# Performance work log

Hardware: AMD Instinct MI355X
Metric: run time of the kernel (lower is better)

Reference implementation:

```python
import jax, jax.numpy as jnp
import numpy as np

N_HEADS = 16
N_KV = 8
HEAD_DIM = 128
HID = 2048
GROUPS = N_HEADS // N_KV
THETA = 10000.0


def _rope_cos_sin(position_ids, dtype):
    # position_ids: [1, S] int
    inv_freq = 1.0 / (THETA ** (jnp.arange(0, HEAD_DIM, 2, dtype=jnp.float32) / HEAD_DIM))
    freqs = position_ids.astype(jnp.float32)[:, :, None] * inv_freq[None, None, :]  # [1,S,hd/2]
    emb = jnp.concatenate([freqs, freqs], axis=-1)  # [1,S,hd]
    return jnp.cos(emb).astype(dtype)[:, None, :, :], jnp.sin(emb).astype(dtype)[:, None, :, :]


def _rotate_half(x):
    x1, x2 = x[..., : HEAD_DIM // 2], x[..., HEAD_DIM // 2 :]
    return jnp.concatenate([-x2, x1], axis=-1)


def setup_inputs() -> dict:
    key = jax.random.key(0)
    ks = jax.random.split(key, 8)
    B, S = 2, 2048
    hidden_states = jax.random.normal(ks[0], (B, S, HID), jnp.float32)
    Wq = jax.random.normal(ks[1], (HID, N_HEADS * HEAD_DIM), jnp.float32) * 0.02
    Wk = jax.random.normal(ks[2], (HID, N_KV * HEAD_DIM), jnp.float32) * 0.02
    Wv = jax.random.normal(ks[3], (HID, N_KV * HEAD_DIM), jnp.float32) * 0.02
    Wo = jax.random.normal(ks[4], (HID, HID), jnp.float32) * 0.02
    gate = jnp.zeros((1, N_HEADS, 1, 1), jnp.float32)
    memory_in = jax.random.normal(ks[5], (B, N_KV, HEAD_DIM, HEAD_DIM), jnp.float32)
    norm_in = jax.random.uniform(ks[6], (B, N_KV, 1, HEAD_DIM), jnp.float32)
    position_ids = jnp.arange(S, dtype=jnp.int32)[None, :]
    return {"hidden_states": hidden_states, "Wq": Wq, "Wk": Wk, "Wv": Wv, "Wo": Wo,
            "gate": gate, "memory_in": memory_in, "norm_in": norm_in,
            "position_ids": position_ids}


def reference(hidden_states, Wq, Wk, Wv, Wo, gate, memory_in, norm_in, position_ids):
    B, S, _ = hidden_states.shape
    # projections -> [B, H, S, hd]
    q = jnp.einsum('bsh,ho->bso', hidden_states, Wq).reshape(B, S, N_HEADS, HEAD_DIM).transpose(0, 2, 1, 3)
    k = jnp.einsum('bsh,ho->bso', hidden_states, Wk).reshape(B, S, N_KV, HEAD_DIM).transpose(0, 2, 1, 3)
    v = jnp.einsum('bsh,ho->bso', hidden_states, Wv).reshape(B, S, N_KV, HEAD_DIM).transpose(0, 2, 1, 3)

    # ---- compressive memory retrieval (pre-RoPE q, as in original) ----
    sigma_q = jax.nn.elu(q) + 1.0  # [B, nH, S, hd]
    mem_tiled = jnp.tile(memory_in, (1, GROUPS, 1, 1))          # torch .repeat tiles
    norm_tiled = jnp.tile(norm_in, (1, GROUPS, 1, 1))            # [B, nH, 1, hd]
    memory_output = jnp.einsum('bhsd,bhde->bhse', sigma_q, mem_tiled)
    norm_bcast = jnp.einsum('bhsd,bhd->bhs', sigma_q, norm_tiled[:, :, 0, :])[..., None]
    memory_output = memory_output / norm_bcast

    # ---- memory update (pre-RoPE k, v) ----
    sigma_k = jax.nn.elu(k) + 1.0  # [B, nKV, S, hd]
    updated_memory = memory_in + jnp.einsum('bhsd,bhse->bhde', sigma_k, v)
    updated_norm = norm_in + jnp.sum(sigma_k, axis=2, keepdims=True)

    # ---- RoPE ----
    cos, sin = _rope_cos_sin(position_ids, q.dtype)
    q = q * cos + _rotate_half(q) * sin
    k = k * cos + _rotate_half(k) * sin

    # ---- repeat_kv (interleave, groups) ----
    k = jnp.repeat(k, GROUPS, axis=1)
    v = jnp.repeat(v, GROUPS, axis=1)

    # ---- causal SDPA ----
    scale = 1.0 / np.sqrt(HEAD_DIM)
    scores = jnp.einsum('bhqd,bhkd->bhqk', q, k) * scale
    causal = jnp.tril(jnp.ones((S, S), dtype=bool))
    scores = jnp.where(causal[None, None], scores, jnp.finfo(scores.dtype).min)
    probs = jax.nn.softmax(scores, axis=-1)
    attn = jnp.einsum('bhqk,bhkd->bhqd', probs, v)

    # ---- gated combination + output projection ----
    g = jax.nn.sigmoid(gate)
    combined = g * memory_output + (1.0 - g) * attn  # [B, nH, S, hd]
    combined = combined.transpose(0, 2, 1, 3).reshape(B, S, HID)
    final_output = jnp.einsum('bsh,ho->bso', combined, Wo)
    return final_output, updated_memory, updated_norm
```

## Files before the change

kernel.cpp:

```cpp
#include <hip/hip_runtime.h>

#define BATCH 2
#define SEQ   2048
#define HID   2048
#define NH    16
#define NKV   8
#define HD    128
#define M_ROWS (BATCH * SEQ)
#define QKV_N  4096

typedef __attribute__((ext_vector_type(8))) __bf16 bf16x8;
typedef __attribute__((ext_vector_type(4))) float  f32x4;

static __device__ __forceinline__ f32x4 mfma16(bf16x8 a, bf16x8 b, f32x4 c) {
    return __builtin_amdgcn_mfma_f32_16x16x32_bf16(a, b, c, 0, 0, 0);
}
static __device__ __forceinline__ float sigma_f(float x) {
    return x > 0.f ? x + 1.f : __expf(x);
}
static __device__ __forceinline__ void gload16(const __bf16* g, __bf16* l) {
    __builtin_amdgcn_global_load_lds(
        (const __attribute__((address_space(1))) void*)g,
        (__attribute__((address_space(3))) void*)l, 16, 0, 0);
}

#define OFF_QKV  0ull
#define OFF_SQ   67108864ull
#define OFF_QR   83886080ull
#define OFF_KR   100663296ull
#define OFF_VT   109051904ull
#define OFF_ND   117440512ull
#define OFF_CB   117702656ull
#define OFF_PART 134479872ull
#define OFF_BND  142868480ull
#define OFF_MAXP 143130624ull
#define OFF_NPART 143134720ull
#define NSPLIT 8

__global__ __launch_bounds__(256) void pre_k(const float* __restrict__ hidden,
                                             const float* __restrict__ Wq,
                                             const float* __restrict__ Wk,
                                             const float* __restrict__ Wv,
                                             __bf16* __restrict__ hb,
                                             __bf16* __restrict__ qkvT)
{
    __shared__ __bf16 T[64][72];
    const int bid = blockIdx.x;
    const int t = threadIdx.x;
    if (bid < 4096) {
        const size_t i = ((size_t)bid * 256 + t) * 8;
        const float4 v0 = *reinterpret_cast<const float4*>(hidden + i);
        const float4 v1 = *reinterpret_cast<const float4*>(hidden + i + 4);
        bf16x8 o;
        o[0]=(__bf16)v0.x; o[1]=(__bf16)v0.y; o[2]=(__bf16)v0.z; o[3]=(__bf16)v0.w;
        o[4]=(__bf16)v1.x; o[5]=(__bf16)v1.y; o[6]=(__bf16)v1.z; o[7]=(__bf16)v1.w;
        *reinterpret_cast<bf16x8*>(hb + i) = o;
        return;
    }
    int tb = bid - 4096;
    const float* W; __bf16* Bt; int N;
    if (tb < 1024)      { W = Wq; Bt = qkvT;                         N = 2048; }
    else if (tb < 1536) { W = Wk; Bt = qkvT + (size_t)2048 * HID;    N = 1024; tb -= 1024; }
    else                { W = Wv; Bt = qkvT + (size_t)3072 * HID;    N = 1024; tb -= 1536; }
    const int k0 = (tb & 31) * 64, n0 = (tb >> 5) * 64;
    #pragma unroll
    for (int i = 0; i < 4; ++i) {
        const int idx = t + i * 256;
        const int r = idx >> 4, c4 = (idx & 15) * 4;
        const float4 v = *reinterpret_cast<const float4*>(&W[(size_t)(k0 + r) * N + n0 + c4]);
        T[c4 + 0][r] = (__bf16)v.x; T[c4 + 1][r] = (__bf16)v.y;
        T[c4 + 2][r] = (__bf16)v.z; T[c4 + 3][r] = (__bf16)v.w;
    }
    __syncthreads();
    #pragma unroll
    for (int i = 0; i < 2; ++i) {
        const int idx = t + i * 256;
        const int rr = idx >> 3, cc = (idx & 7) * 8;
        *reinterpret_cast<bf16x8*>(&Bt[(size_t)(n0 + rr) * HID + k0 + cc]) =
            *reinterpret_cast<bf16x8*>(&T[rr][cc]);
    }
}

__global__ __launch_bounds__(256) void tr_k(const float* __restrict__ W,
                                            __bf16* __restrict__ Bt, int K, int N)
{
    __shared__ __bf16 T[64][72];
    const int k0 = blockIdx.x * 64, n0 = blockIdx.y * 64;
    const int t = threadIdx.x;
    #pragma unroll
    for (int i = 0; i < 4; ++i) {
        const int idx = t + i * 256;
        const int r = idx >> 4, c4 = (idx & 15) * 4;
        const float4 v = *reinterpret_cast<const float4*>(&W[(size_t)(k0 + r) * N + n0 + c4]);
        T[c4 + 0][r] = (__bf16)v.x; T[c4 + 1][r] = (__bf16)v.y;
        T[c4 + 2][r] = (__bf16)v.z; T[c4 + 3][r] = (__bf16)v.w;
    }
    __syncthreads();
    #pragma unroll
    for (int i = 0; i < 2; ++i) {
        const int idx = t + i * 256;
        const int rr = idx >> 3, cc = (idx & 7) * 8;
        *reinterpret_cast<bf16x8*>(&Bt[(size_t)(n0 + rr) * K + k0 + cc]) =
            *reinterpret_cast<bf16x8*>(&T[rr][cc]);
    }
}

__global__ __launch_bounds__(512, 2) void gemm8_k(const __bf16* __restrict__ A,
                                                  const __bf16* __restrict__ Bt,
                                                  float* __restrict__ C,
                                                  int N, int K)
{
    __shared__ __align__(16) __bf16 smem[65536];
    const int tid = threadIdx.x, wave = tid >> 6, lane = tid & 63;
    const int l15 = lane & 15, l4 = lane >> 4;
    const int wr = wave >> 2, wc = wave & 3;

    const int nwg = gridDim.x;
    const int swz = (blockIdx.x & 7) * (nwg >> 3) + (blockIdx.x >> 3);
    const int NBN = N >> 8;
    const int bm = swz / NBN, bn = swz - bm * NBN;
    const int m0 = bm << 8, n0 = bn << 8;

    const int NKT = K >> 6;

    const int srow   = tid >> 2;
    const int schunk = (tid & 3) ^ ((tid >> 3) & 3);
    const int sdst   = wave * 512;

    const int achunk = l4 ^ ((l15 >> 1) & 3);
    const int aoff = (wr * 128 + l15) * 32 + achunk * 8;
    const int boff = (wc * 64  + l15) * 32 + achunk * 8;

    f32x4 acc[2][4][4] = {};
    bf16x8 af[4], bfr[4];

#define STAGE_SLAB(gb, r0, koff, slabptr) do {                                   \
        const __bf16* _g = (gb) + (size_t)((r0) + srow) * K + (koff) + schunk * 8; \
        gload16(_g,                    (slabptr) + sdst);                        \
        gload16(_g + (size_t)128 * K,  (slabptr) + sdst + 4096);                 \
    } while (0)

    STAGE_SLAB(A,  m0, 0,  smem);
    STAGE_SLAB(Bt, n0, 0,  smem + 16384);
    STAGE_SLAB(A,  m0, 32, smem + 8192);
    STAGE_SLAB(Bt, n0, 32, smem + 24576);
    STAGE_SLAB(A,  m0, 64, smem + 32768);
    STAGE_SLAB(Bt, n0, 64, smem + 32768 + 16384);
    asm volatile("s_waitcnt vmcnt(4)" ::: "memory");
    __builtin_amdgcn_s_barrier();

    #pragma unroll 1
    for (int T = 0; T < NKT; ++T) {
        __bf16* bufc = smem + (T & 1) * 32768;
        __bf16* bufn = smem + ((T & 1) ^ 1) * 32768;
        const int kt1 = (T + 1) * 64, kt2 = (T + 2) * 64;

        {
            const __bf16* As = bufc;
            const __bf16* Bs = bufc + 16384;
            #pragma unroll
            for (int f = 0; f < 4; ++f)  af[f]  = *reinterpret_cast<const bf16x8*>(As + aoff + f * 512);
            #pragma unroll
            for (int nf = 0; nf < 4; ++nf) bfr[nf] = *reinterpret_cast<const bf16x8*>(Bs + boff + nf * 512);
            if (T + 1 < NKT) STAGE_SLAB(A, m0, kt1 + 32, bufn + 8192);
            __builtin_amdgcn_s_barrier();
            __builtin_amdgcn_s_setprio(1);
            #pragma unroll
            for (int f = 0; f < 4; ++f)
                #pragma unroll
                for (int nf = 0; nf < 4; ++nf)
                    acc[0][f][nf] = mfma16(af[f], bfr[nf], acc[0][f][nf]);
            __builtin_amdgcn_s_setprio(0);
            __builtin_amdgcn_s_barrier();
        }
        {
            const __bf16* As = bufc;
            #pragma unroll
            for (int f = 0; f < 4; ++f)  af[f] = *reinterpret_cast<const bf16x8*>(As + aoff + 2048 + f * 512);
            if (T + 1 < NKT) STAGE_SLAB(Bt, n0, kt1 + 32, bufn + 24576);
            __builtin_amdgcn_s_barrier();
            __builtin_amdgcn_s_setprio(1);
            #pragma unroll
            for (int f = 0; f < 4; ++f)
                #pragma unroll
                for (int nf = 0; nf < 4; ++nf)
                    acc[1][f][nf] = mfma16(af[f], bfr[nf], acc[1][f][nf]);
            __builtin_amdgcn_s_setprio(0);
            __builtin_amdgcn_s_barrier();
        }
        {
            const __bf16* As = bufc + 8192;
            const __bf16* Bs = bufc + 24576;
            #pragma unroll
            for (int f = 0; f < 4; ++f)  af[f]  = *reinterpret_cast<const bf16x8*>(As + aoff + f * 512);
            #pragma unroll
            for (int nf = 0; nf < 4; ++nf) bfr[nf] = *reinterpret_cast<const bf16x8*>(Bs + boff + nf * 512);
            if (T + 2 < NKT) STAGE_SLAB(A, m0, kt2, bufc);
            __builtin_amdgcn_s_barrier();
            __builtin_amdgcn_s_setprio(1);
            #pragma unroll
            for (int f = 0; f < 4; ++f)
                #pragma unroll
                for (int nf = 0; nf < 4; ++nf)
                    acc[0][f][nf] = mfma16(af[f], bfr[nf], acc[0][f][nf]);
            __builtin_amdgcn_s_setprio(0);
            __builtin_amdgcn_s_barrier();
        }
        {
            const __bf16* As = bufc + 8192;
            #pragma unroll
            for (int f = 0; f < 4; ++f)  af[f] = *reinterpret_cast<const bf16x8*>(As + aoff + 2048 + f * 512);
            if (T + 2 < NKT) STAGE_SLAB(Bt, n0, kt2, bufc + 16384);
            __builtin_amdgcn_s_barrier();
            __builtin_amdgcn_s_setprio(1);
            #pragma unroll
            for (int f = 0; f < 4; ++f)
                #pragma unroll
                for (int nf = 0; nf < 4; ++nf)
                    acc[1][f][nf] = mfma16(af[f], bfr[nf], acc[1][f][nf]);
            __builtin_amdgcn_s_setprio(0);
            if (T < NKT - 2) asm volatile("s_waitcnt vmcnt(4)" ::: "memory");
            else             asm volatile("s_waitcnt vmcnt(0)" ::: "memory");
            __builtin_amdgcn_s_barrier();
        }
    }
#undef STAGE_SLAB

    #pragma unroll
    for (int mh = 0; mh < 2; ++mh)
        #pragma unroll
        for (int f = 0; f < 4; ++f)
            #pragma unroll
            for (int nf = 0; nf < 4; ++nf)
                #pragma unroll
                for (int r = 0; r < 4; ++r) {
                    const int row = m0 + wr * 128 + mh * 64 + f * 16 + l4 * 4 + r;
                    const int col = n0 + wc * 64 + nf * 16 + l15;
                    C[(size_t)row * N + col] = acc[mh][f][nf][r];
                }
}

__global__ __launch_bounds__(512, 2) void gemm8n_k(const __bf16* __restrict__ A,
                                                   const __bf16* __restrict__ Bt,
                                                   float* __restrict__ C,
                                                   int N, int K)
{
    __shared__ __align__(16) __bf16 smem[49152];
    const int tid = threadIdx.x, wave = tid >> 6, lane = tid & 63;
    const int l15 = lane & 15, l4 = lane >> 4;
    const int wr = wave >> 2, wc = wave & 3;

    const int nwg = gridDim.x;
    const int swz = (blockIdx.x & 7) * (nwg >> 3) + (blockIdx.x >> 3);
    const int NBN = N >> 8;
    const int bm = swz / NBN, bn = swz - bm * NBN;
    const int m0 = bm << 7, n0 = bn << 8;

    const int NKT = K >> 6;

    const int srow   = tid >> 2;
    const int schunk = (tid & 3) ^ ((tid >> 3) & 3);
    const int sdst   = wave * 512;

    const int achunk = l4 ^ ((l15 >> 1) & 3);
    const int aoff = (wr * 64 + l15) * 32 + achunk * 8;
    const int boff = (wc * 64 + l15) * 32 + achunk * 8;

    f32x4 acc[4][4] = {};
    bf16x8 af[4], bfr[4];

#define STAGE_A(koff, dstp) do {                                                  \
        gload16(A + (size_t)(m0 + srow) * K + (koff) + schunk * 8, (dstp) + sdst); \
    } while (0)
#define STAGE_B(koff, dstp) do {                                                  \
        const __bf16* _g = Bt + (size_t)(n0 + srow) * K + (koff) + schunk * 8;    \
        gload16(_g,                   (dstp) + sdst);                             \
        gload16(_g + (size_t)128 * K, (dstp) + sdst + 4096);                      \
    } while (0)

    STAGE_A(0,  smem);
    STAGE_B(0,  smem + 8192);
    STAGE_A(32, smem + 4096);
    STAGE_B(32, smem + 16384);
    STAGE_A(64, smem + 24576);
    STAGE_B(64, smem + 24576 + 8192);
    asm volatile("s_waitcnt vmcnt(3)" ::: "memory");
    __builtin_amdgcn_s_barrier();

    #pragma unroll 1
    for (int T = 0; T < NKT; ++T) {
        __bf16* bufc = smem + (T & 1) * 24576;
        __bf16* bufn = smem + ((T & 1) ^ 1) * 24576;
        const int kt1 = (T + 1) * 64, kt2 = (T + 2) * 64;

        {
            #pragma unroll
            for (int f = 0; f < 4; ++f)  af[f]  = *reinterpret_cast<const bf16x8*>(bufc + aoff + f * 512);
            #pragma unroll
            for (int nf = 0; nf < 4; ++nf) bfr[nf] = *reinterpret_cast<const bf16x8*>(bufc + 8192 + boff + nf * 512);
            if (T + 1 < NKT) { STAGE_A(kt1 + 32, bufn + 4096); STAGE_B(kt1 + 32, bufn + 16384); }
            __builtin_amdgcn_s_barrier();
            __builtin_amdgcn_s_setprio(1);
            #pragma unroll
            for (int f = 0; f < 4; ++f)
                #pragma unroll
                for (int nf = 0; nf < 4; ++nf)
                    acc[f][nf] = mfma16(af[f], bfr[nf], acc[f][nf]);
            __builtin_amdgcn_s_setprio(0);
            __builtin_amdgcn_s_barrier();
        }
        {
            #pragma unroll
            for (int f = 0; f < 4; ++f)  af[f]  = *reinterpret_cast<const bf16x8*>(bufc + 4096 + aoff + f * 512);
            #pragma unroll
            for (int nf = 0; nf < 4; ++nf) bfr[nf] = *reinterpret_cast<const bf16x8*>(bufc + 16384 + boff + nf * 512);
            if (T + 2 < NKT) { STAGE_A(kt2, bufc); STAGE_B(kt2, bufc + 8192); }
            __builtin_amdgcn_s_barrier();
            __builtin_amdgcn_s_setprio(1);
            #pragma unroll
            for (int f = 0; f < 4; ++f)
                #pragma unroll
                for (int nf = 0; nf < 4; ++nf)
                    acc[f][nf] = mfma16(af[f], bfr[nf], acc[f][nf]);
            __builtin_amdgcn_s_setprio(0);
            if (T < NKT - 2) asm volatile("s_waitcnt vmcnt(3)" ::: "memory");
            else             asm volatile("s_waitcnt vmcnt(0)" ::: "memory");
            __builtin_amdgcn_s_barrier();
        }
    }
#undef STAGE_A
#undef STAGE_B

    #pragma unroll
    for (int f = 0; f < 4; ++f)
        #pragma unroll
        for (int nf = 0; nf < 4; ++nf)
            #pragma unroll
            for (int r = 0; r < 4; ++r) {
                const int row = m0 + wr * 64 + f * 16 + l4 * 4 + r;
                const int col = n0 + wc * 64 + nf * 16 + l15;
                C[(size_t)row * N + col] = acc[f][nf][r];
            }
}

__global__ __launch_bounds__(256) void prep_k(const float* __restrict__ qkv,
                                              const float* __restrict__ norm_in,
                                              const int* __restrict__ pos_ids,
                                              __bf16* __restrict__ sq, __bf16* __restrict__ qr,
                                              __bf16* __restrict__ kr, __bf16* __restrict__ vt,
                                              float* __restrict__ nd, float* __restrict__ bnd,
                                              float* __restrict__ maxp)
{
    const int sc = blockIdx.x, kvh = blockIdx.y, b = blockIdx.z;
    const int s0 = sc * 32, t = threadIdx.x;
    const float scale = 0.08838834764831845f;
    const float s2 = scale * scale;
    const float NEG_LN_TH = -0.14391156831212787f;
    __shared__ float krn[32];

    {
        const int row = t >> 2;
        const int head = row >> 5, sl = row & 31;
        const int hq = kvh * 2 + head, nh = hq & 7;
        const int dq = (t & 3) * 16;
        const int pos = pos_ids[s0 + sl];
        const float* qp = qkv + (size_t)(b * SEQ + s0 + sl) * QKV_N + hq * 128;
        const float* np = norm_in + (b * NKV + nh) * 128;

        float x0[16], x1[16];
        #pragma unroll
        for (int i = 0; i < 16; i += 4) {
            *reinterpret_cast<float4*>(&x0[i]) = *reinterpret_cast<const float4*>(qp + dq + i);
            *reinterpret_cast<float4*>(&x1[i]) = *reinterpret_cast<const float4*>(qp + dq + 64 + i);
        }
        float nds = 0.f, qns = 0.f;
        bf16x8 sqv0[2], sqv1[2], qrv0[2], qrv1[2];
        #pragma unroll
        for (int i = 0; i < 16; ++i) {
            const int j = dq + i;
            float c, sn;
            __sincosf((float)pos * __expf((float)j * NEG_LN_TH), &sn, &c);
            qrv0[i >> 3][i & 7] = (__bf16)((x0[i] * c - x1[i] * sn) * scale);
            qrv1[i >> 3][i & 7] = (__bf16)((x1[i] * c + x0[i] * sn) * scale);
            const float sg0 = sigma_f(x0[i]), sg1 = sigma_f(x1[i]);
            sqv0[i >> 3][i & 7] = (__bf16)sg0;
            sqv1[i >> 3][i & 7] = (__bf16)sg1;
            nds += sg0 * np[j] + sg1 * np[j + 64];
            qns += (x0[i] * x0[i] + x1[i] * x1[i]) * s2;
        }
        __bf16* sqp = sq + ((size_t)(b * NH + hq) * SEQ + s0 + sl) * 128;
        __bf16* qrp = qr + ((size_t)(b * NH + hq) * SEQ + s0 + sl) * 128;
        *reinterpret_cast<bf16x8*>(sqp + dq)      = sqv0[0];
        *reinterpret_cast<bf16x8*>(sqp + dq + 8)  = sqv0[1];
        *reinterpret_cast<bf16x8*>(sqp + dq + 64) = sqv1[0];
        *reinterpret_cast<bf16x8*>(sqp + dq + 72) = sqv1[1];
        *reinterpret_cast<bf16x8*>(qrp + dq)      = qrv0[0];
        *reinterpret_cast<bf16x8*>(qrp + dq + 8)  = qrv0[1];
        *reinterpret_cast<bf16x8*>(qrp + dq + 64) = qrv1[0];
        *reinterpret_cast<bf16x8*>(qrp + dq + 72) = qrv1[1];

        nds += __shfl_xor(nds, 1); nds += __shfl_xor(nds, 2);
        qns += __shfl_xor(qns, 1); qns += __shfl_xor(qns, 2);
        if ((t & 3) == 0) {
            nd [(size_t)(b * NH + hq) * SEQ + s0 + sl] = nds;
            bnd[(size_t)(b * NH + hq) * SEQ + s0 + sl] = qns;
        }
    }

    if (t < 128) {
        const int sl = t >> 2;
        const int dq = (t & 3) * 16;
        const int pos = pos_ids[s0 + sl];
        const float* kp = qkv + (size_t)(b * SEQ + s0 + sl) * QKV_N + 2048 + kvh * 128;
        float x0[16], x1[16];
        #pragma unroll
        for (int i = 0; i < 16; i += 4) {
            *reinterpret_cast<float4*>(&x0[i]) = *reinterpret_cast<const float4*>(kp + dq + i);
            *reinterpret_cast<float4*>(&x1[i]) = *reinterpret_cast<const float4*>(kp + dq + 64 + i);
        }
        bf16x8 kv0[2], kv1[2];
        float kns = 0.f;
        #pragma unroll
        for (int i = 0; i < 16; ++i) {
            const int j = dq + i;
            float c, sn;
            __sincosf((float)pos * __expf((float)j * NEG_LN_TH), &sn, &c);
            kv0[i >> 3][i & 7] = (__bf16)(x0[i] * c - x1[i] * sn);
            kv1[i >> 3][i & 7] = (__bf16)(x1[i] * c + x0[i] * sn);
            kns += x0[i] * x0[i] + x1[i] * x1[i];
        }
        __bf16* krp = kr + ((size_t)(b * NKV + kvh) * SEQ + s0 + sl) * 128;
        *reinterpret_cast<bf16x8*>(krp + dq)      = kv0[0];
        *reinterpret_cast<bf16x8*>(krp + dq + 8)  = kv0[1];
        *reinterpret_cast<bf16x8*>(krp + dq + 64) = kv1[0];
        *reinterpret_cast<bf16x8*>(krp + dq + 72) = kv1[1];
        kns += __shfl_xor(kns, 1); kns += __shfl_xor(kns, 2);
        if ((t & 3) == 0) krn[sl] = kns;
    }

    __shared__ float vl[128][33];
    {
        const int sl = t >> 3, dch = (t & 7) * 16;
        const float* vp = qkv + (size_t)(b * SEQ + s0 + sl) * QKV_N + 3072 + kvh * 128 + dch;
        float xv[16];
        #pragma unroll
        for (int i = 0; i < 16; i += 4)
            *reinterpret_cast<float4*>(&xv[i]) = *reinterpret_cast<const float4*>(vp + i);
        #pragma unroll
        for (int i = 0; i < 16; ++i) vl[dch + i][sl] = xv[i];
    }
    __syncthreads();
    if (t == 0) {
        float mx = 0.f;
        #pragma unroll
        for (int i = 0; i < 32; ++i) mx = fmaxf(mx, krn[i]);
        maxp[((b * NKV + kvh) << 6) + sc] = mx;
    }
    {
        const int d = t >> 1, sh = (t & 1) * 16;
        bf16x8 o0, o1;
        #pragma unroll
        for (int j = 0; j < 8; ++j) o0[j] = (__bf16)vl[d][sh + j];
        #pragma unroll
        for (int j = 0; j < 8; ++j) o1[j] = (__bf16)vl[d][sh + 8 + j];
        __bf16* vp = vt + ((size_t)((b * NKV + kvh) * 128 + d)) * SEQ + s0 + sh;
        *reinterpret_cast<bf16x8*>(vp)     = o0;
        *reinterpret_cast<bf16x8*>(vp + 8) = o1;
    }
}

__global__ __launch_bounds__(256) void memout_k(const __bf16* __restrict__ sq,
                                                const float* __restrict__ mem_in,
                                                const float* __restrict__ nd,
                                                const float* __restrict__ gate,
                                                __bf16* __restrict__ cb)
{
    __shared__ __align__(16) __bf16 mt[128][136];
    const int tid = threadIdx.x;
    const int h = blockIdx.y, b = blockIdx.z;
    const int s0 = blockIdx.x * 64;

    const float* mem = mem_in + (size_t)(b * NKV + (h & 7)) * 16384;
    for (int i = tid; i < 16384; i += 256) {
        int dd = i >> 7, e = i & 127;
        mt[e][dd] = (__bf16)mem[i];
    }
    __syncthreads();

    const int wave = tid >> 6, lane = tid & 63, l15 = lane & 15, l4 = lane >> 4;
    f32x4 acc[8] = {};
    const __bf16* sqb = sq + ((size_t)(b * NH + h) * SEQ + s0 + wave * 16 + l15) * 128;
    #pragma unroll
    for (int kb = 0; kb < 4; ++kb) {
        bf16x8 a = *reinterpret_cast<const bf16x8*>(sqb + kb * 32 + l4 * 8);
        #pragma unroll
        for (int nc = 0; nc < 8; ++nc) {
            bf16x8 bb = *reinterpret_cast<bf16x8*>(&mt[nc * 16 + l15][kb * 32 + l4 * 8]);
            acc[nc] = mfma16(a, bb, acc[nc]);
        }
    }
    float g = 1.f / (1.f + __expf(-gate[h]));
    #pragma unroll
    for (int r = 0; r < 4; ++r) {
        int srow = s0 + wave * 16 + l4 * 4 + r;
        float scl = g / nd[(size_t)(b * NH + h) * SEQ + srow];
        __bf16* cbp = cb + (size_t)(b * SEQ + srow) * HID + h * 128;
        #pragma unroll
        for (int nc = 0; nc < 8; ++nc)
            cbp[nc * 16 + l15] = (__bf16)(acc[nc][r] * scl);
    }
}

__global__ __launch_bounds__(256) void memupd_k(const float* __restrict__ qkv,
                                                float* __restrict__ part,
                                                float* __restrict__ npart)
{
    const int sp = blockIdx.x, yy = blockIdx.y, b = blockIdx.z;
    const int h = yy & 7, eh = yy >> 3;
    const int tid = threadIdx.x;
    const int tx = tid & 15, ty = tid >> 4;
    __shared__ __align__(16) float sk[8][128];
    __shared__ __align__(16) float sv[8][64];
    float acc[8][4] = {};
    float nacc = 0.f;

    const int s0 = sp * (SEQ / NSPLIT);
    for (int so = 0; so < SEQ / NSPLIT; so += 8) {
        for (int i = tid; i < 8 * 128; i += 256) {
            int rr = i >> 7, dd = i & 127;
            sk[rr][dd] = sigma_f(qkv[(size_t)(b * SEQ + s0 + so + rr) * QKV_N + 2048 + h * 128 + dd]);
        }
        {
            const int rr = tid >> 6, ee = tid & 63;
            const size_t base = (size_t)(b * SEQ + s0 + so) * QKV_N + 3072 + h * 128 + eh * 64 + ee;
            sv[rr][ee]     = qkv[base + (size_t)rr * QKV_N];
            sv[rr + 4][ee] = qkv[base + (size_t)(rr + 4) * QKV_N];
        }
        __syncthreads();
        if (eh == 0 && tid < 128) {
            #pragma unroll
            for (int rr = 0; rr < 8; ++rr) nacc += sk[rr][tid];
        }
        #pragma unroll
        for (int rr = 0; rr < 8; ++rr) {
            float4 k0 = *reinterpret_cast<float4*>(&sk[rr][tx * 8]);
            float4 k1 = *reinterpret_cast<float4*>(&sk[rr][tx * 8 + 4]);
            float4 v0 = *reinterpret_cast<float4*>(&sv[rr][ty * 4]);
            float kreg[8] = {k0.x,k0.y,k0.z,k0.w,k1.x,k1.y,k1.z,k1.w};
            float vreg[4] = {v0.x,v0.y,v0.z,v0.w};
            #pragma unroll
            for (int i = 0; i < 8; ++i)
                #pragma unroll
                for (int j2 = 0; j2 < 4; ++j2)
                    acc[i][j2] += kreg[i] * vreg[j2];
        }
        __syncthreads();
    }
    float* pb = part + ((size_t)sp * (BATCH * NKV) + b * NKV + h) * 16384;
    #pragma unroll
    for (int i = 0; i < 8; ++i) {
        float4 o; o.x = acc[i][0]; o.y = acc[i][1]; o.z = acc[i][2]; o.w = acc[i][3];
        *reinterpret_cast<float4*>(&pb[(tx * 8 + i) * 128 + eh * 64 + ty * 4]) = o;
    }
    if (eh == 0 && tid < 128)
        npart[((size_t)sp * (BATCH * NKV) + b * NKV + h) * 128 + tid] = nacc;
}

__global__ __launch_bounds__(256) void memrednorm_k(const float* __restrict__ part,
                                                    const float* __restrict__ mem_in,
                                                    float* __restrict__ out_mem,
                                                    const float* __restrict__ npart,
                                                    const float* __restrict__ norm_in,
                                                    float* __restrict__ out_norm)
{
    const int bid = blockIdx.x;
    if (bid < 1024) {
        const size_t i = (size_t)bid * 256 + threadIdx.x;
        float a = mem_in[i];
        #pragma unroll
        for (int sp = 0; sp < NSPLIT; ++sp) a += part[(size_t)sp * 262144 + i];
        out_mem[i] = a;
    } else if (threadIdx.x < 128) {
        const int bh = bid - 1024, d = threadIdx.x;
        float a = norm_in[bh * 128 + d];
        #pragma unroll
        for (int sp = 0; sp < NSPLIT; ++sp)
            a += npart[((size_t)sp * (BATCH * NKV) + bh) * 128 + d];
        out_norm[bh * 128 + d] = a;
    }
}

__global__ __launch_bounds__(256, 2) void attn_k(const __bf16* __restrict__ qr,
                                                 const __bf16* __restrict__ kr,
                                                 const __bf16* __restrict__ vt,
                                                 const float* __restrict__ gate,
                                                 const float* __restrict__ bnd,
                                                 const float* __restrict__ maxp,
                                                 __bf16* __restrict__ cb)
{
    __shared__ __align__(16) char smem[81920];
    char* ksB = smem;
    char* vsB = smem + 32768;
    char* pB  = smem + 65536;
    float*  red  = (float*)smem;
    float*  lred = (float*)(smem + 65536);

    const int tid = threadIdx.x, wave = tid >> 6, lane = tid & 63;
    const int l15 = lane & 15, l4 = lane >> 4;
    const int e3 = l15 & 7, e2 = e3 >> 2;
    const int ksub = wave >> 1;
    const int wq   = wave & 1;

    const int n   = blockIdx.x + 16 * (blockIdx.y + 16 * blockIdx.z);
    const int xcd = n & 7, i64 = n >> 3;
    const int grp = xcd * 2 + (i64 >> 5);
    const int within = i64 & 31;
    const int b   = grp >> 3;
    const int kvh = grp & 7;
    const int h   = kvh * 2 + (within >> 4);
    const int x   = within & 15;

    const __bf16* kbase = kr + (size_t)(b * NKV + kvh) * SEQ * 128;
    const __bf16* vbase = vt + (size_t)(b * NKV + kvh) * 128 * SEQ;
    const float* bbase  = bnd + (size_t)(b * NH + h) * SEQ;

    const float g  = 1.f / (1.f + __expf(-gate[h]));
    const float gi = 1.f - g;
    float kn2 = 0.f;
    const float* mp = maxp + (b * NKV + kvh) * 64;
    #pragma unroll
    for (int i = 0; i < 64; i += 4) {
        const float4 v = *reinterpret_cast<const float4*>(mp + i);
        kn2 = fmaxf(kn2, fmaxf(fmaxf(v.x, v.y), fmaxf(v.z, v.w)));
    }
    const float knmax = sqrtf(kn2);

    bf16x8 ones;
    #pragma unroll
    for (int j = 0; j < 8; ++j) ones[j] = (__bf16)1.0f;

    const int srow = wave * 32 + l4;
    const int chA  = (lane & 15) ^ l4;
    const char* KG0 = (const char*)kbase + srow * 256 + chA * 16;
    const char* KG1 = (const char*)kbase + srow * 256 + ((chA ^ 4) * 16);
    const char* VG0 = (const char*)vbase + srow * 4096 + chA * 16;
    const char* VG1 = (const char*)vbase + srow * 4096 + ((chA ^ 4) * 16);
    __bf16* kdst = (__bf16*)(ksB + wave * 8192);
    __bf16* vdst = (__bf16*)(vsB + wave * 8192);

    const int t16 = (l4 ^ (e3 & 3)) * 16;
    const int KBe = l15 * 256 + ksub * 16384 + t16 + e2 * 64;
    const int KBo = l15 * 256 + ksub * 16384 + t16 + (1 ^ e2) * 64;
    const int VB0 = l15 * 256 + t16 + e2 * 64 + ksub * 128;
    const int VB1 = l15 * 256 + t16 + (1 ^ e2) * 64 + ksub * 128;
    const int PWw = wave * 4096 + l4 * 512 + l15 * 2;
    const int PWr = wave * 4096 + l15 * 128 + l4 * 16;

#define ISSUE_K(ktrow) do {                                                      \
        const int _ko = (ktrow) * 256;                                           \
        _Pragma("unroll")                                                        \
        for (int _j = 0; _j < 8; ++_j)                                           \
            gload16((const __bf16*)(((_j & 1) ? KG1 : KG0) + _ko + _j * 1024),   \
                    kdst + _j * 512);                                            \
    } while (0)
#define ISSUE_V(ktrow) do {                                                      \
        const int _vo = (ktrow) * 2;                                             \
        _Pragma("unroll")                                                        \
        for (int _j = 0; _j < 8; ++_j)                                           \
            gload16((const __bf16*)(((_j & 1) ? VG1 : VG0) + _vo + _j * 16384),  \
                    vdst + _j * 512);                                            \
    } while (0)

    #pragma unroll 1
    for (int tile = 0; tile < 2; ++tile) {
        const int q0 = (tile == 0 ? x : 31 - x) * 64;
        const int qw = q0 + wq * 32;
        const int NT = (q0 >> 6) + 1;
        const int NI = (NT + 1) >> 1;

        bf16x8 af[2][4];
        float m_r[2][4];
        #pragma unroll
        for (int m = 0; m < 2; ++m) {
            const __bf16* qb = qr + ((size_t)(b * NH + h) * SEQ + qw + m * 16 + l15) * 128;
            #pragma unroll
            for (int kb = 0; kb < 4; ++kb)
                af[m][kb] = *reinterpret_cast<const bf16x8*>(qb + kb * 32 + l4 * 8);
            #pragma unroll
            for (int r = 0; r < 4; ++r)
                m_r[m][r] = sqrtf(bbase[qw + m * 16 + l4 * 4 + r]) * knmax + 1.0f;
        }

        f32x4 o0[8] = {}, o1[8] = {};
        f32x4 lc0 = {}, lc1 = {};

        ISSUE_K(0);
        ISSUE_V(0);
        asm volatile("s_waitcnt vmcnt(8)" ::: "memory");
        __builtin_amdgcn_sched_barrier(0);
        __builtin_amdgcn_s_barrier();

        #pragma unroll 1
        for (int it = 0; it < NI; ++it) {
            const int s = 2 * it + ksub;
            const bool act  = (s < NT);
            const bool more = (it + 1 < NI);

            f32x4 s0[4] = {}, s1[4] = {};
            if (act) {
                __builtin_amdgcn_s_setprio(1);
                #pragma unroll
                for (int kb = 0; kb < 4; ++kb) {
                    const int kbb = ((kb & 1) ? KBo : KBe) + (kb >> 1) * 128;
                    #pragma unroll
                    for (int sub = 0; sub < 4; ++sub) {
                        bf16x8 bb = *reinterpret_cast<const bf16x8*>(ksB + kbb + sub * 4096);
                        s0[sub] = mfma16(af[0][kb], bb, s0[sub]);
                        s1[sub] = mfma16(af[1][kb], bb, s1[sub]);
                    }
                }
                __builtin_amdgcn_s_setprio(0);
            }
            __builtin_amdgcn_sched_barrier(0);
            __builtin_amdgcn_s_barrier();

            if (more) ISSUE_K((it + 1) * 128);

            if (act) {
                #pragma unroll
                for (int r = 0; r < 4; ++r) {
                    const int q0r = qw + l4 * 4 + r;
                    const int q1r = q0r + 16;
                    #pragma unroll
                    for (int sub = 0; sub < 4; ++sub) {
                        const int key = s * 64 + sub * 16 + l15;
                        float p0 = __expf(s0[sub][r] - m_r[0][r]);
                        float p1 = __expf(s1[sub][r] - m_r[1][r]);
                        p0 = (key <= q0r) ? p0 : 0.f;
                        p1 = (key <= q1r) ? p1 : 0.f;
                        *(__bf16*)(pB + PWw + r * 128 + sub * 32)        = (__bf16)p0;
                        *(__bf16*)(pB + PWw + 2048 + r * 128 + sub * 32) = (__bf16)p1;
                    }
                }
            }
            if (more) asm volatile("s_waitcnt vmcnt(8)" ::: "memory");
            else      asm volatile("s_waitcnt vmcnt(0)" ::: "memory");
            __builtin_amdgcn_sched_barrier(0);
            __builtin_amdgcn_s_barrier();

            if (act) {
                bf16x8 a00 = *reinterpret_cast<const bf16x8*>(pB + PWr);
                bf16x8 a01 = *reinterpret_cast<const bf16x8*>(pB + PWr + 64);
                bf16x8 a10 = *reinterpret_cast<const bf16x8*>(pB + PWr + 2048);
                bf16x8 a11 = *reinterpret_cast<const bf16x8*>(pB + PWr + 2048 + 64);
                __builtin_amdgcn_s_setprio(1);
                lc0 = mfma16(a00, ones, lc0); lc0 = mfma16(a01, ones, lc0);
                lc1 = mfma16(a10, ones, lc1); lc1 = mfma16(a11, ones, lc1);
                #pragma unroll
                for (int nc = 0; nc < 8; ++nc) {
                    bf16x8 b0 = *reinterpret_cast<const bf16x8*>(vsB + VB0 + nc * 4096);
                    bf16x8 b1 = *reinterpret_cast<const bf16x8*>(vsB + VB1 + nc * 4096);
                    o0[nc] = mfma16(a00, b0, o0[nc]); o0[nc] = mfma16(a01, b1, o0[nc]);
                    o1[nc] = mfma16(a10, b0, o1[nc]); o1[nc] = mfma16(a11, b1, o1[nc]);
                }
                __builtin_amdgcn_s_setprio(0);
            }
            __builtin_amdgcn_sched_barrier(0);
            __builtin_amdgcn_s_barrier();

            if (more) {
                ISSUE_V((it + 1) * 128);
                asm volatile("s_waitcnt vmcnt(8)" ::: "memory");
            } else {
                asm volatile("s_waitcnt vmcnt(0)" ::: "memory");
            }
            __builtin_amdgcn_sched_barrier(0);
            __builtin_amdgcn_s_barrier();
        }

        if (wave >= 2) {
            float* rb = red + (wave - 2) * 4224;
            #pragma unroll
            for (int nc = 0; nc < 8; ++nc)
                #pragma unroll
                for (int r = 0; r < 4; ++r) {
                    rb[(l4 * 4 + r) * 132 + nc * 16 + l15]        = o0[nc][r];
                    rb[(16 + l4 * 4 + r) * 132 + nc * 16 + l15]   = o1[nc][r];
                }
            if (l15 == 0) {
                float* lb = lred + (wave - 2) * 32;
                #pragma unroll
                for (int r = 0; r < 4; ++r) {
                    lb[l4 * 4 + r]      = lc0[r];
                    lb[16 + l4 * 4 + r] = lc1[r];
                }
            }
        }
        __syncthreads();
        if (wave < 2) {
            float* rb = red + wave * 4224;
            const float* lb = lred + wave * 32;
            #pragma unroll
            for (int r = 0; r < 4; ++r) {
                const int qrow = qw + l4 * 4 + r;
                const float i0 = gi / (lc0[r] + lb[l4 * 4 + r]);
                const float i1 = gi / (lc1[r] + lb[16 + l4 * 4 + r]);
                __bf16* c0 = cb + (size_t)(b * SEQ + qrow) * HID + h * 128;
                __bf16* c1 = cb + (size_t)(b * SEQ + qrow + 16) * HID + h * 128;
                #pragma unroll
                for (int nc = 0; nc < 8; ++nc) {
                    const int dd = nc * 16 + l15;
                    const float v0 = o0[nc][r] + rb[(l4 * 4 + r) * 132 + dd];
                    const float v1 = o1[nc][r] + rb[(16 + l4 * 4 + r) * 132 + dd];
                    c0[dd] = (__bf16)((float)c0[dd] + v0 * i0);
                    c1[dd] = (__bf16)((float)c1[dd] + v1 * i1);
                }
            }
        }
        __syncthreads();
    }
#undef ISSUE_K
#undef ISSUE_V
}

extern "C" void kernel_launch(void* const* d_in, const int* in_sizes, int n_in,
                              void* d_out, int out_size, void* d_ws, size_t ws_size,
                              hipStream_t stream)
{
    const float* hidden  = (const float*)d_in[0];
    const float* Wq      = (const float*)d_in[1];
    const float* Wk      = (const float*)d_in[2];
    const float* Wv      = (const float*)d_in[3];
    const float* Wo      = (const float*)d_in[4];
    const float* gate    = (const float*)d_in[5];
    const float* mem_in  = (const float*)d_in[6];
    const float* norm_in = (const float*)d_in[7];
    const int*   pos     = (const int*)d_in[8];

    float* out_final = (float*)d_out;
    float* out_mem   = out_final + (size_t)BATCH * SEQ * HID;
    float* out_norm  = out_mem + (size_t)BATCH * NKV * 128 * 128;

    char* ws = (char*)d_ws;
    float*  qkv  = (float*)(ws + OFF_QKV);
    __bf16* sq   = (__bf16*)(ws + OFF_SQ);
    __bf16* qrb  = (__bf16*)(ws + OFF_QR);
    __bf16* krb  = (__bf16*)(ws + OFF_KR);
    __bf16* vtb  = (__bf16*)(ws + OFF_VT);
    float*  nd   = (float*)(ws + OFF_ND);
    __bf16* cb   = (__bf16*)(ws + OFF_CB);
    float*  part = (float*)(ws + OFF_PART);
    float*  bnd  = (float*)(ws + OFF_BND);
    float*  maxp = (float*)(ws + OFF_MAXP);
    float*  npart = (float*)(ws + OFF_NPART);
    __bf16* hb   = (__bf16*)(ws + OFF_SQ);
    __bf16* qkvT = (__bf16*)(ws + OFF_QR);
    __bf16* woT  = (__bf16*)(ws + OFF_PART);

    pre_k<<<6144, 256, 0, stream>>>(hidden, Wq, Wk, Wv, hb, qkvT);

    gemm8_k<<<(M_ROWS / 256) * (QKV_N / 256), 512, 0, stream>>>(hb, qkvT, qkv, QKV_N, HID);

    prep_k<<<dim3(SEQ / 32, NKV, BATCH), 256, 0, stream>>>(qkv, norm_in, pos, sq, qrb, krb, vtb,
                                                           nd, bnd, maxp);

    memout_k<<<dim3(SEQ / 64, NH, BATCH), 256, 0, stream>>>(sq, mem_in, nd, gate, cb);

    memupd_k<<<dim3(NSPLIT, 16, BATCH), 256, 0, stream>>>(qkv, part, npart);
    memrednorm_k<<<1040, 256, 0, stream>>>(part, mem_in, out_mem, npart, norm_in, out_norm);

    tr_k<<<dim3(HID / 64, HID / 64), 256, 0, stream>>>(Wo, woT, HID, HID);

    attn_k<<<dim3(16, NH, BATCH), 256, 0, stream>>>(qrb, krb, vtb, gate, bnd, maxp, cb);

    gemm8n_k<<<(M_ROWS / 128) * (HID / 256), 512, 0, stream>>>(cb, woT, out_final, HID, HID);
}
```

Baseline: 426.4 us.

## Split attention into one query tile per block with smaller K/V tiles for occupancy

The attention kernel used to process two paired causal query tiles per block with 128-key K/V tiles. It now launches twice as many blocks, each handling one 64-row query tile, with 64-key tiles split across wave pairs. Shared memory is halved and launch bounds are raised to allow four blocks per CU. This targets latency hiding and load balance. In exchange it loses the paired-tile balancing, and the smaller tiles mean more barrier iterations per key.

```diff
diff --git a/kernel.cpp b/kernel.cpp
--- a/kernel.cpp
+++ b/kernel.cpp
@@ -590,7 +590,7 @@
     }
 }
 
-__global__ __launch_bounds__(256, 2) void attn_k(const __bf16* __restrict__ qr,
+__global__ __launch_bounds__(256, 4) void attn_k(const __bf16* __restrict__ qr,
                                                  const __bf16* __restrict__ kr,
                                                  const __bf16* __restrict__ vt,
                                                  const float* __restrict__ gate,
@@ -598,27 +598,27 @@
                                                  const float* __restrict__ maxp,
                                                  __bf16* __restrict__ cb)
 {
-    __shared__ __align__(16) char smem[81920];
+    __shared__ __align__(16) char smem[40960];
     char* ksB = smem;
-    char* vsB = smem + 32768;
-    char* pB  = smem + 65536;
+    char* vsB = smem + 16384;
+    char* pB  = smem + 32768;
     float*  red  = (float*)smem;
-    float*  lred = (float*)(smem + 65536);
+    float*  lred = (float*)(smem + 36864);
 
     const int tid = threadIdx.x, wave = tid >> 6, lane = tid & 63;
     const int l15 = lane & 15, l4 = lane >> 4;
     const int e3 = l15 & 7, e2 = e3 >> 2;
-    const int ksub = wave >> 1;
-    const int wq   = wave & 1;
-
-    const int n   = blockIdx.x + 16 * (blockIdx.y + 16 * blockIdx.z);
-    const int xcd = n & 7, i64 = n >> 3;
-    const int grp = xcd * 2 + (i64 >> 5);
-    const int within = i64 & 31;
+    const int kh = wave >> 1;
+    const int wq = wave & 1;
+
+    const int n   = blockIdx.x + 32 * (blockIdx.y + 16 * blockIdx.z);
+    const int xcd = n & 7, i128 = n >> 3;
+    const int grp = xcd * 2 + (i128 >> 6);
+    const int within = i128 & 63;
     const int b   = grp >> 3;
     const int kvh = grp & 7;
-    const int h   = kvh * 2 + (within >> 4);
-    const int x   = within & 15;
+    const int h   = kvh * 2 + (within >> 5);
+    const int x   = 31 - (within & 31);
 
     const __bf16* kbase = kr + (size_t)(b * NKV + kvh) * SEQ * 128;
     const __bf16* vbase = vt + (size_t)(b * NKV + kvh) * 128 * SEQ;
@@ -639,185 +639,171 @@
     #pragma unroll
     for (int j = 0; j < 8; ++j) ones[j] = (__bf16)1.0f;
 
-    const int srow = wave * 32 + l4;
-    const int chA  = (lane & 15) ^ l4;
-    const char* KG0 = (const char*)kbase + srow * 256 + chA * 16;
-    const char* KG1 = (const char*)kbase + srow * 256 + ((chA ^ 4) * 16);
-    const char* VG0 = (const char*)vbase + srow * 4096 + chA * 16;
-    const char* VG1 = (const char*)vbase + srow * 4096 + ((chA ^ 4) * 16);
-    __bf16* kdst = (__bf16*)(ksB + wave * 8192);
-    __bf16* vdst = (__bf16*)(vsB + wave * 8192);
+    const int chA = (lane & 15) ^ l4;
+    const char* KG0 = (const char*)kbase + (wave * 16 + l4) * 256 + chA * 16;
+    const char* KG1 = (const char*)kbase + (wave * 16 + l4) * 256 + ((chA ^ 4) * 16);
+    const int l8 = lane >> 3;
+    const int chV = (lane & 7) ^ (l8 & 7);
+    const char* VG0 = (const char*)vbase + (size_t)(wave * 32 + l8) * 4096 + chV * 16;
+    __bf16* kdst = (__bf16*)(ksB + wave * 4096);
+    __bf16* vdst = (__bf16*)(vsB + wave * 4096);
 
     const int t16 = (l4 ^ (e3 & 3)) * 16;
-    const int KBe = l15 * 256 + ksub * 16384 + t16 + e2 * 64;
-    const int KBo = l15 * 256 + ksub * 16384 + t16 + (1 ^ e2) * 64;
-    const int VB0 = l15 * 256 + t16 + e2 * 64 + ksub * 128;
-    const int VB1 = l15 * 256 + t16 + (1 ^ e2) * 64 + ksub * 128;
-    const int PWw = wave * 4096 + l4 * 512 + l15 * 2;
-    const int PWr = wave * 4096 + l15 * 128 + l4 * 16;
+    const int KBe = l15 * 256 + kh * 8192 + t16 + e2 * 64;
+    const int KBo = l15 * 256 + kh * 8192 + t16 + (1 ^ e2) * 64;
+    const int VB  = l15 * 128 + t16 + ((kh ^ e2) * 64);
+    const int PWw = wave * 2048 + l15 * 2;
+    const int PWr = wave * 2048 + l15 * 64 + l4 * 16;
 
 #define ISSUE_K(ktrow) do {                                                      \
         const int _ko = (ktrow) * 256;                                           \
-        _Pragma("unroll")                                                        \
-        for (int _j = 0; _j < 8; ++_j)                                           \
-            gload16((const __bf16*)(((_j & 1) ? KG1 : KG0) + _ko + _j * 1024),   \
-                    kdst + _j * 512);                                            \
+        gload16((const __bf16*)(KG0 + _ko),        kdst);                        \
+        gload16((const __bf16*)(KG1 + _ko + 1024), kdst + 512);                  \
+        gload16((const __bf16*)(KG0 + _ko + 2048), kdst + 1024);                 \
+        gload16((const __bf16*)(KG1 + _ko + 3072), kdst + 1536);                 \
     } while (0)
 #define ISSUE_V(ktrow) do {                                                      \
         const int _vo = (ktrow) * 2;                                             \
-        _Pragma("unroll")                                                        \
-        for (int _j = 0; _j < 8; ++_j)                                           \
-            gload16((const __bf16*)(((_j & 1) ? VG1 : VG0) + _vo + _j * 16384),  \
-                    vdst + _j * 512);                                            \
+        gload16((const __bf16*)(VG0 + _vo),         vdst);                       \
+        gload16((const __bf16*)(VG0 + _vo + 32768), vdst + 512);                 \
+        gload16((const __bf16*)(VG0 + _vo + 65536), vdst + 1024);                \
+        gload16((const __bf16*)(VG0 + _vo + 98304), vdst + 1536);                \
     } while (0)
 
+    const int q0 = x * 64;
+    const int qw = q0 + wq * 32;
+    const int NT = (q0 >> 6) + 1;
+
+    bf16x8 af[2][4];
+    float m_r[2][4];
+    #pragma unroll
+    for (int m = 0; m < 2; ++m) {
+        const __bf16* qb = qr + ((size_t)(b * NH + h) * SEQ + qw + m * 16 + l15) * 128;
+        #pragma unroll
+        for (int kb = 0; kb < 4; ++kb)
+            af[m][kb] = *reinterpret_cast<const bf16x8*>(qb + kb * 32 + l4 * 8);
+        #pragma unroll
+        for (int r = 0; r < 4; ++r)
+            m_r[m][r] = sqrtf(bbase[qw + m * 16 + l4 * 4 + r]) * knmax + 1.0f;
+    }
+
+    f32x4 o0[8] = {}, o1[8] = {};
+    f32x4 lc0 = {}, lc1 = {};
+
+    ISSUE_K(0);
+    ISSUE_V(0);
+    asm volatile("s_waitcnt vmcnt(4)" ::: "memory");
+    __builtin_amdgcn_sched_barrier(0);
+    __builtin_amdgcn_s_barrier();
+
     #pragma unroll 1
-    for (int tile = 0; tile < 2; ++tile) {
-        const int q0 = (tile == 0 ? x : 31 - x) * 64;
-        const int qw = q0 + wq * 32;
-        const int NT = (q0 >> 6) + 1;
-        const int NI = (NT + 1) >> 1;
-
-        bf16x8 af[2][4];
-        float m_r[2][4];
-        #pragma unroll
-        for (int m = 0; m < 2; ++m) {
-            const __bf16* qb = qr + ((size_t)(b * NH + h) * SEQ + qw + m * 16 + l15) * 128;
-            #pragma unroll
-            for (int kb = 0; kb < 4; ++kb)
-                af[m][kb] = *reinterpret_cast<const bf16x8*>(qb + kb * 32 + l4 * 8);
-            #pragma unroll
-            for (int r = 0; r < 4; ++r)
-                m_r[m][r] = sqrtf(bbase[qw + m * 16 + l4 * 4 + r]) * knmax + 1.0f;
-        }
-
-        f32x4 o0[8] = {}, o1[8] = {};
-        f32x4 lc0 = {}, lc1 = {};
-
-        ISSUE_K(0);
-        ISSUE_V(0);
-        asm volatile("s_waitcnt vmcnt(8)" ::: "memory");
+    for (int it = 0; it < NT; ++it) {
+        const bool more = (it + 1 < NT);
+
+        f32x4 s0[2] = {}, s1[2] = {};
+        __builtin_amdgcn_s_setprio(1);
+        #pragma unroll
+        for (int kb = 0; kb < 4; ++kb) {
+            const int kbb = ((kb & 1) ? KBo : KBe) + (kb >> 1) * 128;
+            #pragma unroll
+            for (int sub = 0; sub < 2; ++sub) {
+                bf16x8 bb = *reinterpret_cast<const bf16x8*>(ksB + kbb + sub * 4096);
+                s0[sub] = mfma16(af[0][kb], bb, s0[sub]);
+                s1[sub] = mfma16(af[1][kb], bb, s1[sub]);
+            }
+        }
+        __builtin_amdgcn_s_setprio(0);
         __builtin_amdgcn_sched_barrier(0);
         __builtin_amdgcn_s_barrier();
 
-        #pragma unroll 1
-        for (int it = 0; it < NI; ++it) {
-            const int s = 2 * it + ksub;
-            const bool act  = (s < NT);
-            const bool more = (it + 1 < NI);
-
-            f32x4 s0[4] = {}, s1[4] = {};
-            if (act) {
-                __builtin_amdgcn_s_setprio(1);
-                #pragma unroll
-                for (int kb = 0; kb < 4; ++kb) {
-                    const int kbb = ((kb & 1) ? KBo : KBe) + (kb >> 1) * 128;
-                    #pragma unroll
-                    for (int sub = 0; sub < 4; ++sub) {
-                        bf16x8 bb = *reinterpret_cast<const bf16x8*>(ksB + kbb + sub * 4096);
-                        s0[sub] = mfma16(af[0][kb], bb, s0[sub]);
-                        s1[sub] = mfma16(af[1][kb], bb, s1[sub]);
-                    }
-                }
-                __builtin_amdgcn_s_setprio(0);
+        if (more) ISSUE_K((it + 1) * 64);
+
+        #pragma unroll
+        for (int r = 0; r < 4; ++r) {
+            const int q0r = qw + l4 * 4 + r;
+            const int q1r = q0r + 16;
+            const int rw = PWw + (l4 * 4 + r) * 64;
+            #pragma unroll
+            for (int sub = 0; sub < 2; ++sub) {
+                const int key = it * 64 + kh * 32 + sub * 16 + l15;
+                float p0 = __expf(s0[sub][r] - m_r[0][r]);
+                float p1 = __expf(s1[sub][r] - m_r[1][r]);
+                p0 = (key <= q0r) ? p0 : 0.f;
+                p1 = (key <= q1r) ? p1 : 0.f;
+                *(__bf16*)(pB + rw + sub * 32)        = (__bf16)p0;
+                *(__bf16*)(pB + rw + 1024 + sub * 32) = (__bf16)p1;
             }
-            __builtin_amdgcn_sched_barrier(0);
-            __builtin_amdgcn_s_barrier();
-
-            if (more) ISSUE_K((it + 1) * 128);
-
-            if (act) {
-                #pragma unroll
-                for (int r = 0; r < 4; ++r) {
-                    const int q0r = qw + l4 * 4 + r;
-                    const int q1r = q0r + 16;
-                    #pragma unroll
-                    for (int sub = 0; sub < 4; ++sub) {
-                        const int key = s * 64 + sub * 16 + l15;
-                        float p0 = __expf(s0[sub][r] - m_r[0][r]);
-                        float p1 = __expf(s1[sub][r] - m_r[1][r]);
-                        p0 = (key <= q0r) ? p0 : 0.f;
-                        p1 = (key <= q1r) ? p1 : 0.f;
-                        *(__bf16*)(pB + PWw + r * 128 + sub * 32)        = (__bf16)p0;
-                        *(__bf16*)(pB + PWw + 2048 + r * 128 + sub * 32) = (__bf16)p1;
-                    }
-                }
+        }
+        if (more) asm volatile("s_waitcnt vmcnt(4)" ::: "memory");
+        else      asm volatile("s_waitcnt vmcnt(0)" ::: "memory");
+        __builtin_amdgcn_sched_barrier(0);
+        __builtin_amdgcn_s_barrier();
+
+        {
+            bf16x8 a0 = *reinterpret_cast<const bf16x8*>(pB + PWr);
+            bf16x8 a1 = *reinterpret_cast<const bf16x8*>(pB + PWr + 1024);
+            __builtin_amdgcn_s_setprio(1);
+            lc0 = mfma16(a0, ones, lc0);
+            lc1 = mfma16(a1, ones, lc1);
+            #pragma unroll
+            for (int nc = 0; nc < 8; ++nc) {
+                bf16x8 b0 = *reinterpret_cast<const bf16x8*>(vsB + VB + nc * 2048);
+                o0[nc] = mfma16(a0, b0, o0[nc]);
+                o1[nc] = mfma16(a1, b0, o1[nc]);
             }
-            if (more) asm volatile("s_waitcnt vmcnt(8)" ::: "memory");
-            else      asm volatile("s_waitcnt vmcnt(0)" ::: "memory");
-            __builtin_amdgcn_sched_barrier(0);
-            __builtin_amdgcn_s_barrier();
-
-            if (act) {
-                bf16x8 a00 = *reinterpret_cast<const bf16x8*>(pB + PWr);
-                bf16x8 a01 = *reinterpret_cast<const bf16x8*>(pB + PWr + 64);
-                bf16x8 a10 = *reinterpret_cast<const bf16x8*>(pB + PWr + 2048);
-                bf16x8 a11 = *reinterpret_cast<const bf16x8*>(pB + PWr + 2048 + 64);
-                __builtin_amdgcn_s_setprio(1);
-                lc0 = mfma16(a00, ones, lc0); lc0 = mfma16(a01, ones, lc0);
-                lc1 = mfma16(a10, ones, lc1); lc1 = mfma16(a11, ones, lc1);
-                #pragma unroll
-                for (int nc = 0; nc < 8; ++nc) {
-                    bf16x8 b0 = *reinterpret_cast<const bf16x8*>(vsB + VB0 + nc * 4096);
-                    bf16x8 b1 = *reinterpret_cast<const bf16x8*>(vsB + VB1 + nc * 4096);
-                    o0[nc] = mfma16(a00, b0, o0[nc]); o0[nc] = mfma16(a01, b1, o0[nc]);
-                    o1[nc] = mfma16(a10, b0, o1[nc]); o1[nc] = mfma16(a11, b1, o1[nc]);
-                }
-                __builtin_amdgcn_s_setprio(0);
+            __builtin_amdgcn_s_setprio(0);
+        }
+        __builtin_amdgcn_sched_barrier(0);
+        __builtin_amdgcn_s_barrier();
+
+        if (more) {
+            ISSUE_V((it + 1) * 64);
+            asm volatile("s_waitcnt vmcnt(4)" ::: "memory");
+        } else {
+            asm volatile("s_waitcnt vmcnt(0)" ::: "memory");
+        }
+        __builtin_amdgcn_sched_barrier(0);
+        __builtin_amdgcn_s_barrier();
+    }
+
+    if (wave >= 2) {
+        float* rb = red + (wave - 2) * 4224;
+        #pragma unroll
+        for (int nc = 0; nc < 8; ++nc)
+            #pragma unroll
+            for (int r = 0; r < 4; ++r) {
+                rb[(l4 * 4 + r) * 132 + nc * 16 + l15]        = o0[nc][r];
+                rb[(16 + l4 * 4 + r) * 132 + nc * 16 + l15]   = o1[nc][r];
             }
-            __builtin_amdgcn_sched_barrier(0);
-            __builtin_amdgcn_s_barrier();
-
-            if (more) {
-                ISSUE_V((it + 1) * 128);
-                asm volatile("s_waitcnt vmcnt(8)" ::: "memory");
-            } else {
-                asm volatile("s_waitcnt vmcnt(0)" ::: "memory");
+        if (l15 == 0) {
+            float* lb = lred + (wave - 2) * 32;
+            #pragma unroll
+            for (int r = 0; r < 4; ++r) {
+                lb[l4 * 4 + r]      = lc0[r];
+                lb[16 + l4 * 4 + r] = lc1[r];
             }
-            __builtin_amdgcn_sched_barrier(0);
-            __builtin_amdgcn_s_barrier();
-        }
-
-        if (wave >= 2) {
-            float* rb = red + (wave - 2) * 4224;
-            #pragma unroll
-            for (int nc = 0; nc < 8; ++nc)
-                #pragma unroll
-                for (int r = 0; r < 4; ++r) {
-                    rb[(l4 * 4 + r) * 132 + nc * 16 + l15]        = o0[nc][r];
-                    rb[(16 + l4 * 4 + r) * 132 + nc * 16 + l15]   = o1[nc][r];
-                }
-            if (l15 == 0) {
-                float* lb = lred + (wave - 2) * 32;
-                #pragma unroll
-                for (int r = 0; r < 4; ++r) {
-                    lb[l4 * 4 + r]      = lc0[r];
-                    lb[16 + l4 * 4 + r] = lc1[r];
-                }
+        }
+    }
+    __syncthreads();
+    if (wave < 2) {
+        float* rb = red + wave * 4224;
+        const float* lb = lred + wave * 32;
+        #pragma unroll
+        for (int r = 0; r < 4; ++r) {
+            const int qrow = qw + l4 * 4 + r;
+            const float i0 = gi / (lc0[r] + lb[l4 * 4 + r]);
+            const float i1 = gi / (lc1[r] + lb[16 + l4 * 4 + r]);
+            __bf16* c0 = cb + (size_t)(b * SEQ + qrow) * HID + h * 128;
+            __bf16* c1 = cb + (size_t)(b * SEQ + qrow + 16) * HID + h * 128;
+            #pragma unroll
+            for (int nc = 0; nc < 8; ++nc) {
+                const int dd = nc * 16 + l15;
+                const float v0 = o0[nc][r] + rb[(l4 * 4 + r) * 132 + dd];
+                const float v1 = o1[nc][r] + rb[(16 + l4 * 4 + r) * 132 + dd];
+                c0[dd] = (__bf16)((float)c0[dd] + v0 * i0);
+                c1[dd] = (__bf16)((float)c1[dd] + v1 * i1);
             }
         }
-        __syncthreads();
-        if (wave < 2) {
-            float* rb = red + wave * 4224;
-            const float* lb = lred + wave * 32;
-            #pragma unroll
-            for (int r = 0; r < 4; ++r) {
-                const int qrow = qw + l4 * 4 + r;
-                const float i0 = gi / (lc0[r] + lb[l4 * 4 + r]);
-                const float i1 = gi / (lc1[r] + lb[16 + l4 * 4 + r]);
-                __bf16* c0 = cb + (size_t)(b * SEQ + qrow) * HID + h * 128;
-                __bf16* c1 = cb + (size_t)(b * SEQ + qrow + 16) * HID + h * 128;
-                #pragma unroll
-                for (int nc = 0; nc < 8; ++nc) {
-                    const int dd = nc * 16 + l15;
-                    const float v0 = o0[nc][r] + rb[(l4 * 4 + r) * 132 + dd];
-                    const float v1 = o1[nc][r] + rb[(16 + l4 * 4 + r) * 132 + dd];
-                    c0[dd] = (__bf16)((float)c0[dd] + v0 * i0);
-                    c1[dd] = (__bf16)((float)c1[dd] + v1 * i1);
-                }
-            }
-        }
-        __syncthreads();
     }
 #undef ISSUE_K
 #undef ISSUE_V
@@ -871,7 +857,7 @@
 
     tr_k<<<dim3(HID / 64, HID / 64), 256, 0, stream>>>(Wo, woT, HID, HID);
 
-    attn_k<<<dim3(16, NH, BATCH), 256, 0, stream>>>(qrb, krb, vtb, gate, bnd, maxp, cb);
+    attn_k<<<dim3(32, NH, BATCH), 256, 0, stream>>>(qrb, krb, vtb, gate, bnd, maxp, cb);
 
     gemm8n_k<<<(M_ROWS / 128) * (HID / 256), 512, 0, stream>>>(cb, woT, out_final, HID, HID);
 }
```

Result: slower. 592.0 us (+38.9%).
